# Optimization experiments

Measured on AMD Instinct MI355X. Metric: run time of the kernel, lower is better.

The kernel has to match this reference:

```python
import jax, jax.numpy as jnp
import numpy as np

B, S, D = 2, 2048, 4096
H = 32
HD = D // H  # 128
THETA = 10000.0


def _rope_cos_sin(seq_len, head_dim, theta=THETA):
    # matches precompute_freqs_cis: freqs_cis[t, j] = exp(i * t * theta**(-2j/dim))
    inv = 1.0 / theta ** (np.arange(0, head_dim, 2)[: head_dim // 2].astype(np.float32) / head_dim)
    t = np.arange(seq_len)
    f = np.outer(t, inv).astype(np.float32)  # [S, HD/2]
    return jnp.asarray(np.cos(f)), jnp.asarray(np.sin(f))


def _apply_rotary(x, cos, sin):
    # x: [B, S, H, HD]; interleaved complex rotation as in apply_rotary_emb
    xr = x.astype(jnp.float32).reshape(*x.shape[:-1], HD // 2, 2)
    x0, x1 = xr[..., 0], xr[..., 1]
    c = cos[None, :, None, :]  # [1,S,1,HD/2]
    s = sin[None, :, None, :]
    o0 = x0 * c - x1 * s
    o1 = x0 * s + x1 * c
    return jnp.stack((o0, o1), axis=-1).reshape(*x.shape[:-1], HD)


def setup_inputs() -> dict:
    key = jax.random.key(0)
    ks = jax.random.split(key, 5)
    std = 0.02
    return {
        "x": jax.random.normal(ks[0], (B, S, D), dtype=jnp.float32),
        "wq": jax.random.normal(ks[1], (D, D), dtype=jnp.float32) * std,
        "wk": jax.random.normal(ks[2], (D, D), dtype=jnp.float32) * std,
        "wv": jax.random.normal(ks[3], (D, D), dtype=jnp.float32) * std,
        "wo": jax.random.normal(ks[4], (D, D), dtype=jnp.float32) * std,
    }


def reference(x, wq, wk, wv, wo):
    b, s, d = x.shape
    q = (x @ wq).reshape(b, s, H, HD)
    k = (x @ wk).reshape(b, s, H, HD)
    v = (x @ wv).reshape(b, s, H, HD)

    cos, sin = _rope_cos_sin(s, HD)
    q = _apply_rotary(q, cos, sin)
    k = _apply_rotary(k, cos, sin)

    scale = 1.0 / jnp.sqrt(jnp.float32(HD))
    scores = jnp.einsum("bqhd,bkhd->bhqk", q, k) * scale  # [B,H,S,S]
    causal = jnp.tril(jnp.ones((s, s), dtype=bool))
    scores = jnp.where(causal[None, None], scores, jnp.finfo(scores.dtype).min)
    probs = jax.nn.softmax(scores, axis=-1)
    out = jnp.einsum("bhqk,bkhd->bqhd", probs, v).reshape(b, s, d)
    return out @ wo
```

## Files before the change

kernel.cpp:

```cpp
#include <hip/hip_runtime.h>

#define DEV __device__ __forceinline__
typedef unsigned int u32;
typedef unsigned short u16;
typedef __attribute__((ext_vector_type(8))) __bf16 bf16x8;
typedef __attribute__((ext_vector_type(4))) float f32x4;

#define MFMA16(a,b,c) __builtin_amdgcn_mfma_f32_16x16x32_bf16(a,b,c,0,0,0)

DEV u16 f2bf(float f){ u32 u=__float_as_uint(f); u32 r=(u+0x7fffu+((u>>16)&1u))>>16; return (u16)r; }
DEV float bf2f(u16 h){ return __uint_as_float(((u32)h)<<16); }

DEV void gload16(const void* g, void* l){
  __builtin_amdgcn_global_load_lds((const __attribute__((address_space(1))) void*)g,
                                   (__attribute__((address_space(3))) void*)l, 16, 0, 0);
}


template<bool SPLIT>
__global__ void k_split(const float* __restrict__ in, u16* __restrict__ hi, u16* __restrict__ lo){
  size_t i=((size_t)blockIdx.x*256+threadIdx.x)*4;
  float4 v=*(const float4*)(in+i);
  u16 h0=f2bf(v.x),h1=f2bf(v.y),h2=f2bf(v.z),h3=f2bf(v.w);
  uint2 hh; hh.x=(u32)h0|((u32)h1<<16); hh.y=(u32)h2|((u32)h3<<16);
  *(uint2*)(hi+i)=hh;
  if constexpr(SPLIT){
    uint2 ll; ll.x=(u32)f2bf(v.x-bf2f(h0))|((u32)f2bf(v.y-bf2f(h1))<<16);
    ll.y=(u32)f2bf(v.z-bf2f(h2))|((u32)f2bf(v.w-bf2f(h3))<<16);
    *(uint2*)(lo+i)=ll;
  }
}

template<bool SPLIT>
__global__ void k_trans_split(const float* __restrict__ W, u16* __restrict__ hiT, u16* __restrict__ loT){
  __shared__ float t[64][65];
  const int tid=threadIdx.x;
  const int kb=blockIdx.y*64, nb=blockIdx.x*64;
  for(int p=0;p<4;p++){
    int r=(tid>>4)+p*16, c=(tid&15)*4;
    float4 v=*(const float4*)(W+(size_t)(kb+r)*4096+nb+c);
    t[r][c]=v.x;t[r][c+1]=v.y;t[r][c+2]=v.z;t[r][c+3]=v.w;
  }
  __syncthreads();
  for(int p=0;p<4;p++){
    int orow=(tid>>4)+p*16, oc=(tid&15)*4;
    u16 hs[4],ls[4];
    for(int j=0;j<4;j++){
      float x=t[oc+j][orow];
      hs[j]=f2bf(x); ls[j]=f2bf(x-bf2f(hs[j]));
    }
    uint2 uh; uh.x=(u32)hs[0]|((u32)hs[1]<<16); uh.y=(u32)hs[2]|((u32)hs[3]<<16);
    *(uint2*)(hiT+(size_t)(nb+orow)*4096+kb+oc)=uh;
    if constexpr(SPLIT){
      uint2 ul; ul.x=(u32)ls[0]|((u32)ls[1]<<16); ul.y=(u32)ls[2]|((u32)ls[3]<<16);
      *(uint2*)(loT+(size_t)(nb+orow)*4096+kb+oc)=ul;
    }
  }
}

__global__ void k_rope_tab(float* __restrict__ cosT, float* __restrict__ sinT){
  int i=blockIdx.x*256+threadIdx.x;
  int s=i>>6, f=i&63;
  float inv=powf(10000.f, -(float)(2*f)/128.f);
  float ang=(float)s*inv;
  cosT[i]=cosf(ang); sinT[i]=sinf(ang);
}

template<int EPI, bool SPLIT>
__global__ __launch_bounds__(256,2) void k_gemm(
    const u16* __restrict__ Ah, const u16* __restrict__ Al,
    const u16* __restrict__ Bh, const u16* __restrict__ Bl,
    float* __restrict__ outF, u16* __restrict__ outH, u16* __restrict__ outL,
    const float* __restrict__ cosT, const float* __restrict__ sinT)
{
  __shared__ u16 lds[4][4096];
  const int tid=threadIdx.x, lane=tid&63, w=tid>>6;
  const int m0=blockIdx.y*128, n0=blockIdx.x*128;
  const int wm=(w>>1)*64, wn=(w&1)*64;
  const f32x4 zero4={0.f,0.f,0.f,0.f};
  f32x4 acc[4][4];
  for(int m=0;m<4;m++)for(int n=0;n<4;n++)acc[m][n]=zero4;
  const int srow=lane>>2, soff=(lane&3)*8;
  for(int k0=0;k0<4096;k0+=32){
    for(int q8=w;q8<8;q8+=4){
      int r=q8*16+srow;
      size_t ao=(size_t)(m0+r)*4096+k0+soff;
      size_t bo=(size_t)(n0+r)*4096+k0+soff;
      gload16(Ah+ao,(char*)&lds[0][0]+q8*1024);
      gload16(Bh+bo,(char*)&lds[2][0]+q8*1024);
      if constexpr(SPLIT){
        gload16(Al+ao,(char*)&lds[1][0]+q8*1024);
        gload16(Bl+bo,(char*)&lds[3][0]+q8*1024);
      }
    }
    __syncthreads();
    const int fr=lane&15, fo=(lane>>4)*8;
    bf16x8 ah[4],al[4],bh[4],bl[4];
    for(int m=0;m<4;m++){
      int r=wm+m*16+fr;
      ah[m]=*(const bf16x8*)&lds[0][r*32+fo];
      if constexpr(SPLIT) al[m]=*(const bf16x8*)&lds[1][r*32+fo];
    }
    for(int n=0;n<4;n++){
      int r=wn+n*16+fr;
      bh[n]=*(const bf16x8*)&lds[2][r*32+fo];
      if constexpr(SPLIT) bl[n]=*(const bf16x8*)&lds[3][r*32+fo];
    }
    for(int m=0;m<4;m++)for(int n=0;n<4;n++){
      f32x4 c=acc[m][n];
      c=MFMA16(ah[m],bh[n],c);
      if constexpr(SPLIT){
        c=MFMA16(ah[m],bl[n],c);
        c=MFMA16(al[m],bh[n],c);
      }
      acc[m][n]=c;
    }
    __syncthreads();
  }
  for(int m=0;m<4;m++)for(int n=0;n<4;n++){
    int col=n0+wn+n*16+(lane&15);
    for(int r=0;r<4;r++){
      int row=m0+wm+m*16+(lane>>4)*4+r;
      float v=acc[m][n][r];
      if constexpr(EPI==1){
        int b=row>>11, s=row&2047, hd=col&127, hh=col>>7;
        float part=__shfl_xor(v,1);
        int fi=hd>>1;
        float cs=cosT[s*64+fi], sn=sinT[s*64+fi];
        float o=(hd&1)?(part*sn+v*cs):(v*cs-part*sn);
        u16 hb=f2bf(o);
        size_t addr=((size_t)(b*32+hh)*2048+s)*128+hd;
        outH[addr]=hb;
        if constexpr(SPLIT) outL[addr]=f2bf(o-bf2f(hb));
      } else if constexpr(EPI==2){
        u16 hb=f2bf(v);
        size_t addr=(size_t)row*4096+col;
        outH[addr]=hb;
        if constexpr(SPLIT) outL[addr]=f2bf(v-bf2f(hb));
      } else {
        outF[(size_t)row*4096+col]=v;
      }
    }
  }
}

template<bool SPLIT>
__global__ __launch_bounds__(256,2) void k_attn(
    const u16* __restrict__ Qh, const u16* __restrict__ Ql,
    const u16* __restrict__ Kh, const u16* __restrict__ Kl,
    const u16* __restrict__ VTh, const u16* __restrict__ VTl,
    u16* __restrict__ Oh, u16* __restrict__ Ol)
{
  __shared__ u16 kvh[8192], kvl[8192];
  __shared__ u16 pbuf[4][2][1024];
  const int tid=threadIdx.x, lane=tid&63, w=tid>>6;
  const int q0=blockIdx.x*64, hh=blockIdx.y, b=blockIdx.z;
  const size_t headoff=((size_t)(b*32+hh))*2048*128;
  bf16x8 qh[4],ql[4];
  {
    int qr=q0+w*16+(lane&15);
    for(int c=0;c<4;c++){
      size_t a=headoff+(size_t)qr*128+(lane>>4)*8+32*c;
      qh[c]=*(const bf16x8*)(Qh+a);
      if constexpr(SPLIT) ql[c]=*(const bf16x8*)(Ql+a);
    }
  }
  const f32x4 zero4={0.f,0.f,0.f,0.f};
  f32x4 O[8]; for(int i=0;i<8;i++)O[i]=zero4;
  float m_run=-__builtin_inff(), l_run=0.f;
  const int nt=q0/64+1;
  const int qg=q0+w*16+(lane&15);
  const float scale=0.08838834764831845f;
  for(int t=0;t<nt;t++){
    const int kv0=t*64;
    for(int ch=w*4;ch<w*4+4;++ch){
      int p=ch*1024+lane*16;
      int row=p>>8, slot=(p>>4)&15, ss=slot^(row&7);
      size_t src=headoff+(size_t)(kv0+row)*128+ss*8;
      gload16(Kh+src,(char*)kvh+ch*1024);
      if constexpr(SPLIT) gload16(Kl+src,(char*)kvl+ch*1024);
    }
    __syncthreads();
    f32x4 st[4]; for(int m=0;m<4;m++)st[m]=zero4;
    for(int c=0;c<4;c++){
      for(int m=0;m<4;m++){
        int row=m*16+(lane&15);
        int off=(((lane>>4)*16)+64*c)^((row&7)<<4);
        bf16x8 k8h=*(const bf16x8*)((const char*)kvh+row*256+off);
        st[m]=MFMA16(k8h,qh[c],st[m]);
        if constexpr(SPLIT){
          bf16x8 k8l=*(const bf16x8*)((const char*)kvl+row*256+off);
          st[m]=MFMA16(k8h,ql[c],st[m]);
          st[m]=MFMA16(k8l,qh[c],st[m]);
        }
      }
    }
    __syncthreads();
    for(int ch=w*4;ch<w*4+4;++ch){
      int p=ch*1024+lane*16;
      int row=p>>7, slot=(p>>4)&7, ps=slot^(row&7);
      size_t src=(size_t)(hh*128+row)*4096+(size_t)b*2048+kv0+ps*8;
      gload16(VTh+src,(char*)kvh+ch*1024);
      if constexpr(SPLIT) gload16(VTl+src,(char*)kvl+ch*1024);
    }
    float pm=-__builtin_inff();
    for(int m=0;m<4;m++)for(int r=0;r<4;r++){
      float sv=st[m][r]*scale;
      int kv=kv0+m*16+(lane>>4)*4+r;
      if(kv>qg)sv=-__builtin_inff();
      st[m][r]=sv;
      pm=fmaxf(pm,sv);
    }
    pm=fmaxf(pm,__shfl_xor(pm,16));
    pm=fmaxf(pm,__shfl_xor(pm,32));
    float m_new=fmaxf(m_run,pm);
    float corr=__expf(m_run-m_new);
    float psum=0.f;
    for(int m=0;m<4;m++){
      u16 ph[4],pl[4];
      for(int r=0;r<4;r++){
        float p=__expf(st[m][r]-m_new);
        psum+=p;
        ph[r]=f2bf(p); pl[r]=f2bf(p-bf2f(ph[r]));
      }
      int q=lane&15;
      int off=((m*32)+((lane>>4)*8))^((q&7)<<4);
      uint2 uh; uh.x=(u32)ph[0]|((u32)ph[1]<<16); uh.y=(u32)ph[2]|((u32)ph[3]<<16);
      *(uint2*)((char*)&pbuf[w][0][0]+q*128+off)=uh;
      if constexpr(SPLIT){
        uint2 ul; ul.x=(u32)pl[0]|((u32)pl[1]<<16); ul.y=(u32)pl[2]|((u32)pl[3]<<16);
        *(uint2*)((char*)&pbuf[w][1][0]+q*128+off)=ul;
      }
    }
    psum+=__shfl_xor(psum,16);
    psum+=__shfl_xor(psum,32);
    l_run=l_run*corr+psum;
    m_run=m_new;
    float cb[4];
    for(int r=0;r<4;r++)cb[r]=__shfl(corr,(lane>>4)*4+r);
    for(int nb=0;nb<8;nb++)for(int r=0;r<4;r++)O[nb][r]*=cb[r];
    __syncthreads();
    for(int c2=0;c2<2;c2++){
      int q=lane&15;
      int offp=(((lane>>4)*16)+64*c2)^((q&7)<<4);
      bf16x8 pah=*(const bf16x8*)((const char*)&pbuf[w][0][0]+q*128+offp);
      for(int nb=0;nb<8;nb++){
        int vrow=nb*16+(lane&15);
        int voff=(((lane>>4)*16)+64*c2)^((vrow&7)<<4);
        bf16x8 v8h=*(const bf16x8*)((const char*)kvh+vrow*128+voff);
        O[nb]=MFMA16(pah,v8h,O[nb]);
        if constexpr(SPLIT){
          bf16x8 pal=*(const bf16x8*)((const char*)&pbuf[w][1][0]+q*128+offp);
          bf16x8 v8l=*(const bf16x8*)((const char*)kvl+vrow*128+voff);
          O[nb]=MFMA16(pah,v8l,O[nb]);
          O[nb]=MFMA16(pal,v8h,O[nb]);
        }
      }
    }
    __syncthreads();
  }
  float lb[4];
  for(int r=0;r<4;r++)lb[r]=__shfl(l_run,(lane>>4)*4+r);
  for(int nb=0;nb<8;nb++){
    int col=hh*128+nb*16+(lane&15);
    for(int r=0;r<4;r++){
      float o=O[nb][r]/lb[r];
      size_t rowg=(size_t)b*2048+q0+w*16+(lane>>4)*4+r;
      u16 hb=f2bf(o);
      Oh[rowg*4096+col]=hb;
      if constexpr(SPLIT) Ol[rowg*4096+col]=f2bf(o-bf2f(hb));
    }
  }
}

extern "C" void kernel_launch(void* const* d_in, const int* in_sizes, int n_in,
                              void* d_out, int out_size, void* d_ws, size_t ws_size,
                              hipStream_t stream){
  (void)in_sizes;(void)n_in;(void)out_size;
  const float* x =(const float*)d_in[0];
  const float* wq=(const float*)d_in[1];
  const float* wk=(const float*)d_in[2];
  const float* wv=(const float*)d_in[3];
  const float* wo=(const float*)d_in[4];
  const size_t NELEM=(size_t)4096*4096;
  const size_t MAT=NELEM*sizeof(u16);
  const size_t TAB=(size_t)2048*64*sizeof(float);
  const size_t need_split=10*MAT+2*TAB;
  const size_t need_bf16 = 5*MAT+2*TAB;
  if(ws_size<need_bf16)return;
  const bool split = ws_size>=need_split;
  char* ws=(char*)d_ws;
  size_t off=0;
  auto alloc=[&](size_t bytes)->char*{ char* p=ws+off; off+=bytes; return p; };
  auto allocOpt=[&](size_t bytes)->char*{ if(!split)return nullptr; char* p=ws+off; off+=bytes; return p; };
  u16* x_hi=(u16*)alloc(MAT);   u16* x_lo=(u16*)allocOpt(MAT);
  u16* w_hi=(u16*)alloc(MAT);   u16* w_lo=(u16*)allocOpt(MAT);
  u16* q_hi=(u16*)alloc(MAT);   u16* q_lo=(u16*)allocOpt(MAT);
  u16* k_hi=(u16*)alloc(MAT);   u16* k_lo=(u16*)allocOpt(MAT);
  u16* vT_hi=(u16*)alloc(MAT);  u16* vT_lo=(u16*)allocOpt(MAT);
  float* cosT=(float*)alloc(TAB);
  float* sinT=(float*)alloc(TAB);
  u16* at_hi=x_hi;  u16* at_lo=x_lo;

  dim3 tg(64,64), gg(32,32), ga(32,32,2);
  k_rope_tab<<<512,256,0,stream>>>(cosT,sinT);
  if(split){
    k_split<true><<<(u32)(NELEM/1024),256,0,stream>>>(x,x_hi,x_lo);
    k_trans_split<true><<<tg,256,0,stream>>>(wq,w_hi,w_lo);
    k_gemm<1,true><<<gg,256,0,stream>>>(x_hi,x_lo,w_hi,w_lo,nullptr,q_hi,q_lo,cosT,sinT);
    k_trans_split<true><<<tg,256,0,stream>>>(wk,w_hi,w_lo);
    k_gemm<1,true><<<gg,256,0,stream>>>(x_hi,x_lo,w_hi,w_lo,nullptr,k_hi,k_lo,cosT,sinT);
    k_trans_split<true><<<tg,256,0,stream>>>(wv,w_hi,w_lo);
    k_gemm<2,true><<<gg,256,0,stream>>>(w_hi,w_lo,x_hi,x_lo,nullptr,vT_hi,vT_lo,nullptr,nullptr);
    k_attn<true><<<ga,256,0,stream>>>(q_hi,q_lo,k_hi,k_lo,vT_hi,vT_lo,at_hi,at_lo);
    k_trans_split<true><<<tg,256,0,stream>>>(wo,w_hi,w_lo);
    k_gemm<3,true><<<gg,256,0,stream>>>(at_hi,at_lo,w_hi,w_lo,(float*)d_out,nullptr,nullptr,nullptr,nullptr);
  } else {
    k_split<false><<<(u32)(NELEM/1024),256,0,stream>>>(x,x_hi,nullptr);
    k_trans_split<false><<<tg,256,0,stream>>>(wq,w_hi,nullptr);
    k_gemm<1,false><<<gg,256,0,stream>>>(x_hi,nullptr,w_hi,nullptr,nullptr,q_hi,nullptr,cosT,sinT);
    k_trans_split<false><<<tg,256,0,stream>>>(wk,w_hi,nullptr);
    k_gemm<1,false><<<gg,256,0,stream>>>(x_hi,nullptr,w_hi,nullptr,nullptr,k_hi,nullptr,cosT,sinT);
    k_trans_split<false><<<tg,256,0,stream>>>(wv,w_hi,nullptr);
    k_gemm<2,false><<<gg,256,0,stream>>>(w_hi,nullptr,x_hi,nullptr,nullptr,vT_hi,nullptr,nullptr,nullptr);
    k_attn<false><<<ga,256,0,stream>>>(q_hi,nullptr,k_hi,nullptr,vT_hi,nullptr,at_hi,nullptr);
    k_trans_split<false><<<tg,256,0,stream>>>(wo,w_hi,nullptr);
    k_gemm<3,false><<<gg,256,0,stream>>>(at_hi,nullptr,w_hi,nullptr,(float*)d_out,nullptr,nullptr,nullptr,nullptr);
  }
}
```

Measured before the change: 1.150 ms.

## Replace split-bf16 three-pass MFMA with single-pass fp16 throughout

Drops the hi/lo bf16 split emulation of fp32 and uses plain fp16 operands with a single MFMA per tile in the GEMMs and attention. This cuts matrix-core work, halves LDS and global traffic, and removes the split/residual conversion kernels. The attention kernel also raises its occupancy hint and reverses the query-block order so the longest causal blocks start first. The risk is accuracy: fp16 has fewer mantissa bits than split-bf16 and can overflow on large values.

```diff
diff --git a/kernel.cpp b/kernel.cpp
--- a/kernel.cpp
+++ b/kernel.cpp
@@ -3,13 +3,12 @@
 #define DEV __device__ __forceinline__
 typedef unsigned int u32;
 typedef unsigned short u16;
-typedef __attribute__((ext_vector_type(8))) __bf16 bf16x8;
+typedef __attribute__((ext_vector_type(8))) _Float16 f16x8;
 typedef __attribute__((ext_vector_type(4))) float f32x4;
 
-#define MFMA16(a,b,c) __builtin_amdgcn_mfma_f32_16x16x32_bf16(a,b,c,0,0,0)
-
-DEV u16 f2bf(float f){ u32 u=__float_as_uint(f); u32 r=(u+0x7fffu+((u>>16)&1u))>>16; return (u16)r; }
-DEV float bf2f(u16 h){ return __uint_as_float(((u32)h)<<16); }
+#define MFMA16(a,b,c) __builtin_amdgcn_mfma_f32_16x16x32_f16(a,b,c,0,0,0)
+
+DEV u16 f2h(float f){ _Float16 h=(_Float16)f; return __builtin_bit_cast(u16,h); }
 
 DEV void gload16(const void* g, void* l){
   __builtin_amdgcn_global_load_lds((const __attribute__((address_space(1))) void*)g,
@@ -17,22 +16,14 @@
 }
 
 
-template<bool SPLIT>
-__global__ void k_split(const float* __restrict__ in, u16* __restrict__ hi, u16* __restrict__ lo){
+__global__ void k_cvt(const float* __restrict__ in, u16* __restrict__ out){
   size_t i=((size_t)blockIdx.x*256+threadIdx.x)*4;
   float4 v=*(const float4*)(in+i);
-  u16 h0=f2bf(v.x),h1=f2bf(v.y),h2=f2bf(v.z),h3=f2bf(v.w);
-  uint2 hh; hh.x=(u32)h0|((u32)h1<<16); hh.y=(u32)h2|((u32)h3<<16);
-  *(uint2*)(hi+i)=hh;
-  if constexpr(SPLIT){
-    uint2 ll; ll.x=(u32)f2bf(v.x-bf2f(h0))|((u32)f2bf(v.y-bf2f(h1))<<16);
-    ll.y=(u32)f2bf(v.z-bf2f(h2))|((u32)f2bf(v.w-bf2f(h3))<<16);
-    *(uint2*)(lo+i)=ll;
-  }
-}
-
-template<bool SPLIT>
-__global__ void k_trans_split(const float* __restrict__ W, u16* __restrict__ hiT, u16* __restrict__ loT){
+  uint2 hh; hh.x=(u32)f2h(v.x)|((u32)f2h(v.y)<<16); hh.y=(u32)f2h(v.z)|((u32)f2h(v.w)<<16);
+  *(uint2*)(out+i)=hh;
+}
+
+__global__ void k_trans(const float* __restrict__ W, u16* __restrict__ outT){
   __shared__ float t[64][65];
   const int tid=threadIdx.x;
   const int kb=blockIdx.y*64, nb=blockIdx.x*64;
@@ -44,17 +35,10 @@
   __syncthreads();
   for(int p=0;p<4;p++){
     int orow=(tid>>4)+p*16, oc=(tid&15)*4;
-    u16 hs[4],ls[4];
-    for(int j=0;j<4;j++){
-      float x=t[oc+j][orow];
-      hs[j]=f2bf(x); ls[j]=f2bf(x-bf2f(hs[j]));
-    }
+    u16 hs[4];
+    for(int j=0;j<4;j++) hs[j]=f2h(t[oc+j][orow]);
     uint2 uh; uh.x=(u32)hs[0]|((u32)hs[1]<<16); uh.y=(u32)hs[2]|((u32)hs[3]<<16);
-    *(uint2*)(hiT+(size_t)(nb+orow)*4096+kb+oc)=uh;
-    if constexpr(SPLIT){
-      uint2 ul; ul.x=(u32)ls[0]|((u32)ls[1]<<16); ul.y=(u32)ls[2]|((u32)ls[3]<<16);
-      *(uint2*)(loT+(size_t)(nb+orow)*4096+kb+oc)=ul;
-    }
+    *(uint2*)(outT+(size_t)(nb+orow)*4096+kb+oc)=uh;
   }
 }
 
@@ -66,14 +50,13 @@
   cosT[i]=cosf(ang); sinT[i]=sinf(ang);
 }
 
-template<int EPI, bool SPLIT>
+template<int EPI>
 __global__ __launch_bounds__(256,2) void k_gemm(
-    const u16* __restrict__ Ah, const u16* __restrict__ Al,
-    const u16* __restrict__ Bh, const u16* __restrict__ Bl,
-    float* __restrict__ outF, u16* __restrict__ outH, u16* __restrict__ outL,
+    const u16* __restrict__ A, const u16* __restrict__ B,
+    float* __restrict__ outF, u16* __restrict__ outH,
     const float* __restrict__ cosT, const float* __restrict__ sinT)
 {
-  __shared__ u16 lds[4][4096];
+  __shared__ u16 lds[2][4096];
   const int tid=threadIdx.x, lane=tid&63, w=tid>>6;
   const int m0=blockIdx.y*128, n0=blockIdx.x*128;
   const int wm=(w>>1)*64, wn=(w&1)*64;
@@ -84,37 +67,16 @@
   for(int k0=0;k0<4096;k0+=32){
     for(int q8=w;q8<8;q8+=4){
       int r=q8*16+srow;
-      size_t ao=(size_t)(m0+r)*4096+k0+soff;
-      size_t bo=(size_t)(n0+r)*4096+k0+soff;
-      gload16(Ah+ao,(char*)&lds[0][0]+q8*1024);
-      gload16(Bh+bo,(char*)&lds[2][0]+q8*1024);
-      if constexpr(SPLIT){
-        gload16(Al+ao,(char*)&lds[1][0]+q8*1024);
-        gload16(Bl+bo,(char*)&lds[3][0]+q8*1024);
-      }
+      gload16(A+(size_t)(m0+r)*4096+k0+soff,(char*)&lds[0][0]+q8*1024);
+      gload16(B+(size_t)(n0+r)*4096+k0+soff,(char*)&lds[1][0]+q8*1024);
     }
     __syncthreads();
     const int fr=lane&15, fo=(lane>>4)*8;
-    bf16x8 ah[4],al[4],bh[4],bl[4];
-    for(int m=0;m<4;m++){
-      int r=wm+m*16+fr;
-      ah[m]=*(const bf16x8*)&lds[0][r*32+fo];
-      if constexpr(SPLIT) al[m]=*(const bf16x8*)&lds[1][r*32+fo];
-    }
-    for(int n=0;n<4;n++){
-      int r=wn+n*16+fr;
-      bh[n]=*(const bf16x8*)&lds[2][r*32+fo];
-      if constexpr(SPLIT) bl[n]=*(const bf16x8*)&lds[3][r*32+fo];
-    }
-    for(int m=0;m<4;m++)for(int n=0;n<4;n++){
-      f32x4 c=acc[m][n];
-      c=MFMA16(ah[m],bh[n],c);
-      if constexpr(SPLIT){
-        c=MFMA16(ah[m],bl[n],c);
-        c=MFMA16(al[m],bh[n],c);
-      }
-      acc[m][n]=c;
-    }
+    f16x8 ah[4],bh[4];
+    for(int m=0;m<4;m++) ah[m]=*(const f16x8*)&lds[0][(wm+m*16+fr)*32+fo];
+    for(int n=0;n<4;n++) bh[n]=*(const f16x8*)&lds[1][(wn+n*16+fr)*32+fo];
+    for(int m=0;m<4;m++)for(int n=0;n<4;n++)
+      acc[m][n]=MFMA16(ah[m],bh[n],acc[m][n]);
     __syncthreads();
   }
   for(int m=0;m<4;m++)for(int n=0;n<4;n++){
@@ -128,15 +90,10 @@
         int fi=hd>>1;
         float cs=cosT[s*64+fi], sn=sinT[s*64+fi];
         float o=(hd&1)?(part*sn+v*cs):(v*cs-part*sn);
-        u16 hb=f2bf(o);
         size_t addr=((size_t)(b*32+hh)*2048+s)*128+hd;
-        outH[addr]=hb;
-        if constexpr(SPLIT) outL[addr]=f2bf(o-bf2f(hb));
+        outH[addr]=f2h(o);
       } else if constexpr(EPI==2){
-        u16 hb=f2bf(v);
-        size_t addr=(size_t)row*4096+col;
-        outH[addr]=hb;
-        if constexpr(SPLIT) outL[addr]=f2bf(v-bf2f(hb));
+        outH[(size_t)row*4096+col]=f2h(v);
       } else {
         outF[(size_t)row*4096+col]=v;
       }
@@ -144,26 +101,21 @@
   }
 }
 
-template<bool SPLIT>
-__global__ __launch_bounds__(256,2) void k_attn(
-    const u16* __restrict__ Qh, const u16* __restrict__ Ql,
-    const u16* __restrict__ Kh, const u16* __restrict__ Kl,
-    const u16* __restrict__ VTh, const u16* __restrict__ VTl,
-    u16* __restrict__ Oh, u16* __restrict__ Ol)
+__global__ __launch_bounds__(256,4) void k_attn(
+    const u16* __restrict__ Q, const u16* __restrict__ K,
+    const u16* __restrict__ VT, u16* __restrict__ Oat)
 {
-  __shared__ u16 kvh[8192], kvl[8192];
-  __shared__ u16 pbuf[4][2][1024];
+  __shared__ u16 kv[8192];
+  __shared__ u16 pbuf[4][1024];
   const int tid=threadIdx.x, lane=tid&63, w=tid>>6;
-  const int q0=blockIdx.x*64, hh=blockIdx.y, b=blockIdx.z;
+  const int q0=(31-(int)blockIdx.x)*64;
+  const int hh=blockIdx.y, b=blockIdx.z;
   const size_t headoff=((size_t)(b*32+hh))*2048*128;
-  bf16x8 qh[4],ql[4];
+  f16x8 qh[4];
   {
     int qr=q0+w*16+(lane&15);
-    for(int c=0;c<4;c++){
-      size_t a=headoff+(size_t)qr*128+(lane>>4)*8+32*c;
-      qh[c]=*(const bf16x8*)(Qh+a);
-      if constexpr(SPLIT) ql[c]=*(const bf16x8*)(Ql+a);
-    }
+    for(int c=0;c<4;c++)
+      qh[c]=*(const f16x8*)(Q+headoff+(size_t)qr*128+(lane>>4)*8+32*c);
   }
   const f32x4 zero4={0.f,0.f,0.f,0.f};
   f32x4 O[8]; for(int i=0;i<8;i++)O[i]=zero4;
@@ -176,9 +128,7 @@
     for(int ch=w*4;ch<w*4+4;++ch){
       int p=ch*1024+lane*16;
       int row=p>>8, slot=(p>>4)&15, ss=slot^(row&7);
-      size_t src=headoff+(size_t)(kv0+row)*128+ss*8;
-      gload16(Kh+src,(char*)kvh+ch*1024);
-      if constexpr(SPLIT) gload16(Kl+src,(char*)kvl+ch*1024);
+      gload16(K+headoff+(size_t)(kv0+row)*128+ss*8,(char*)kv+ch*1024);
     }
     __syncthreads();
     f32x4 st[4]; for(int m=0;m<4;m++)st[m]=zero4;
@@ -186,28 +136,21 @@
       for(int m=0;m<4;m++){
         int row=m*16+(lane&15);
         int off=(((lane>>4)*16)+64*c)^((row&7)<<4);
-        bf16x8 k8h=*(const bf16x8*)((const char*)kvh+row*256+off);
-        st[m]=MFMA16(k8h,qh[c],st[m]);
-        if constexpr(SPLIT){
-          bf16x8 k8l=*(const bf16x8*)((const char*)kvl+row*256+off);
-          st[m]=MFMA16(k8h,ql[c],st[m]);
-          st[m]=MFMA16(k8l,qh[c],st[m]);
-        }
+        f16x8 k8=*(const f16x8*)((const char*)kv+row*256+off);
+        st[m]=MFMA16(k8,qh[c],st[m]);
       }
     }
     __syncthreads();
     for(int ch=w*4;ch<w*4+4;++ch){
       int p=ch*1024+lane*16;
       int row=p>>7, slot=(p>>4)&7, ps=slot^(row&7);
-      size_t src=(size_t)(hh*128+row)*4096+(size_t)b*2048+kv0+ps*8;
-      gload16(VTh+src,(char*)kvh+ch*1024);
-      if constexpr(SPLIT) gload16(VTl+src,(char*)kvl+ch*1024);
+      gload16(VT+(size_t)(hh*128+row)*4096+(size_t)b*2048+kv0+ps*8,(char*)kv+ch*1024);
     }
     float pm=-__builtin_inff();
     for(int m=0;m<4;m++)for(int r=0;r<4;r++){
       float sv=st[m][r]*scale;
-      int kv=kv0+m*16+(lane>>4)*4+r;
-      if(kv>qg)sv=-__builtin_inff();
+      int kvi=kv0+m*16+(lane>>4)*4+r;
+      if(kvi>qg)sv=-__builtin_inff();
       st[m][r]=sv;
       pm=fmaxf(pm,sv);
     }
@@ -216,21 +159,17 @@
     float m_new=fmaxf(m_run,pm);
     float corr=__expf(m_run-m_new);
     float psum=0.f;
+    const int q=lane&15;
     for(int m=0;m<4;m++){
-      u16 ph[4],pl[4];
+      u16 ph[4];
       for(int r=0;r<4;r++){
         float p=__expf(st[m][r]-m_new);
         psum+=p;
-        ph[r]=f2bf(p); pl[r]=f2bf(p-bf2f(ph[r]));
-      }
-      int q=lane&15;
+        ph[r]=f2h(p);
+      }
       int off=((m*32)+((lane>>4)*8))^((q&7)<<4);
       uint2 uh; uh.x=(u32)ph[0]|((u32)ph[1]<<16); uh.y=(u32)ph[2]|((u32)ph[3]<<16);
-      *(uint2*)((char*)&pbuf[w][0][0]+q*128+off)=uh;
-      if constexpr(SPLIT){
-        uint2 ul; ul.x=(u32)pl[0]|((u32)pl[1]<<16); ul.y=(u32)pl[2]|((u32)pl[3]<<16);
-        *(uint2*)((char*)&pbuf[w][1][0]+q*128+off)=ul;
-      }
+      *(uint2*)((char*)&pbuf[w][0]+q*128+off)=uh;
     }
     psum+=__shfl_xor(psum,16);
     psum+=__shfl_xor(psum,32);
@@ -241,20 +180,13 @@
     for(int nb=0;nb<8;nb++)for(int r=0;r<4;r++)O[nb][r]*=cb[r];
     __syncthreads();
     for(int c2=0;c2<2;c2++){
-      int q=lane&15;
       int offp=(((lane>>4)*16)+64*c2)^((q&7)<<4);
-      bf16x8 pah=*(const bf16x8*)((const char*)&pbuf[w][0][0]+q*128+offp);
+      f16x8 pa=*(const f16x8*)((const char*)&pbuf[w][0]+q*128+offp);
       for(int nb=0;nb<8;nb++){
         int vrow=nb*16+(lane&15);
         int voff=(((lane>>4)*16)+64*c2)^((vrow&7)<<4);
-        bf16x8 v8h=*(const bf16x8*)((const char*)kvh+vrow*128+voff);
-        O[nb]=MFMA16(pah,v8h,O[nb]);
-        if constexpr(SPLIT){
-          bf16x8 pal=*(const bf16x8*)((const char*)&pbuf[w][1][0]+q*128+offp);
-          bf16x8 v8l=*(const bf16x8*)((const char*)kvl+vrow*128+voff);
-          O[nb]=MFMA16(pah,v8l,O[nb]);
-          O[nb]=MFMA16(pal,v8h,O[nb]);
-        }
+        f16x8 v8=*(const f16x8*)((const char*)kv+vrow*128+voff);
+        O[nb]=MFMA16(pa,v8,O[nb]);
       }
     }
     __syncthreads();
@@ -266,9 +198,7 @@
     for(int r=0;r<4;r++){
       float o=O[nb][r]/lb[r];
       size_t rowg=(size_t)b*2048+q0+w*16+(lane>>4)*4+r;
-      u16 hb=f2bf(o);
-      Oh[rowg*4096+col]=hb;
-      if constexpr(SPLIT) Ol[rowg*4096+col]=f2bf(o-bf2f(hb));
+      Oat[rowg*4096+col]=f2h(o);
     }
   }
 }
@@ -285,46 +215,30 @@
   const size_t NELEM=(size_t)4096*4096;
   const size_t MAT=NELEM*sizeof(u16);
   const size_t TAB=(size_t)2048*64*sizeof(float);
-  const size_t need_split=10*MAT+2*TAB;
-  const size_t need_bf16 = 5*MAT+2*TAB;
-  if(ws_size<need_bf16)return;
-  const bool split = ws_size>=need_split;
+  const size_t need=5*MAT+2*TAB;
+  if(ws_size<need)return;
   char* ws=(char*)d_ws;
   size_t off=0;
   auto alloc=[&](size_t bytes)->char*{ char* p=ws+off; off+=bytes; return p; };
-  auto allocOpt=[&](size_t bytes)->char*{ if(!split)return nullptr; char* p=ws+off; off+=bytes; return p; };
-  u16* x_hi=(u16*)alloc(MAT);   u16* x_lo=(u16*)allocOpt(MAT);
-  u16* w_hi=(u16*)alloc(MAT);   u16* w_lo=(u16*)allocOpt(MAT);
-  u16* q_hi=(u16*)alloc(MAT);   u16* q_lo=(u16*)allocOpt(MAT);
-  u16* k_hi=(u16*)alloc(MAT);   u16* k_lo=(u16*)allocOpt(MAT);
-  u16* vT_hi=(u16*)alloc(MAT);  u16* vT_lo=(u16*)allocOpt(MAT);
+  u16* x_h =(u16*)alloc(MAT);
+  u16* w_h =(u16*)alloc(MAT);
+  u16* q_h =(u16*)alloc(MAT);
+  u16* k_h =(u16*)alloc(MAT);
+  u16* vT_h=(u16*)alloc(MAT);
   float* cosT=(float*)alloc(TAB);
   float* sinT=(float*)alloc(TAB);
-  u16* at_hi=x_hi;  u16* at_lo=x_lo;
+  u16* at_h=x_h;
 
   dim3 tg(64,64), gg(32,32), ga(32,32,2);
   k_rope_tab<<<512,256,0,stream>>>(cosT,sinT);
-  if(split){
-    k_split<true><<<(u32)(NELEM/1024),256,0,stream>>>(x,x_hi,x_lo);
-    k_trans_split<true><<<tg,256,0,stream>>>(wq,w_hi,w_lo);
-    k_gemm<1,true><<<gg,256,0,stream>>>(x_hi,x_lo,w_hi,w_lo,nullptr,q_hi,q_lo,cosT,sinT);
-    k_trans_split<true><<<tg,256,0,stream>>>(wk,w_hi,w_lo);
-    k_gemm<1,true><<<gg,256,0,stream>>>(x_hi,x_lo,w_hi,w_lo,nullptr,k_hi,k_lo,cosT,sinT);
-    k_trans_split<true><<<tg,256,0,stream>>>(wv,w_hi,w_lo);
-    k_gemm<2,true><<<gg,256,0,stream>>>(w_hi,w_lo,x_hi,x_lo,nullptr,vT_hi,vT_lo,nullptr,nullptr);
-    k_attn<true><<<ga,256,0,stream>>>(q_hi,q_lo,k_hi,k_lo,vT_hi,vT_lo,at_hi,at_lo);
-    k_trans_split<true><<<tg,256,0,stream>>>(wo,w_hi,w_lo);
-    k_gemm<3,true><<<gg,256,0,stream>>>(at_hi,at_lo,w_hi,w_lo,(float*)d_out,nullptr,nullptr,nullptr,nullptr);
-  } else {
-    k_split<false><<<(u32)(NELEM/1024),256,0,stream>>>(x,x_hi,nullptr);
-    k_trans_split<false><<<tg,256,0,stream>>>(wq,w_hi,nullptr);
-    k_gemm<1,false><<<gg,256,0,stream>>>(x_hi,nullptr,w_hi,nullptr,nullptr,q_hi,nullptr,cosT,sinT);
-    k_trans_split<false><<<tg,256,0,stream>>>(wk,w_hi,nullptr);
-    k_gemm<1,false><<<gg,256,0,stream>>>(x_hi,nullptr,w_hi,nullptr,nullptr,k_hi,nullptr,cosT,sinT);
-    k_trans_split<false><<<tg,256,0,stream>>>(wv,w_hi,nullptr);
-    k_gemm<2,false><<<gg,256,0,stream>>>(w_hi,nullptr,x_hi,nullptr,nullptr,vT_hi,nullptr,nullptr,nullptr);
-    k_attn<false><<<ga,256,0,stream>>>(q_hi,nullptr,k_hi,nullptr,vT_hi,nullptr,at_hi,nullptr);
-    k_trans_split<false><<<tg,256,0,stream>>>(wo,w_hi,nullptr);
-    k_gemm<3,false><<<gg,256,0,stream>>>(at_hi,nullptr,w_hi,nullptr,(float*)d_out,nullptr,nullptr,nullptr,nullptr);
-  }
-}
+  k_cvt<<<(u32)(NELEM/1024),256,0,stream>>>(x,x_h);
+  k_trans<<<tg,256,0,stream>>>(wq,w_h);
+  k_gemm<1><<<gg,256,0,stream>>>(x_h,w_h,nullptr,q_h,cosT,sinT);
+  k_trans<<<tg,256,0,stream>>>(wk,w_h);
+  k_gemm<1><<<gg,256,0,stream>>>(x_h,w_h,nullptr,k_h,cosT,sinT);
+  k_trans<<<tg,256,0,stream>>>(wv,w_h);
+  k_gemm<2><<<gg,256,0,stream>>>(w_h,x_h,nullptr,vT_h,nullptr,nullptr);
+  k_attn<<<ga,256,0,stream>>>(q_h,k_h,vT_h,at_h);
+  k_trans<<<tg,256,0,stream>>>(wo,w_h);
+  k_gemm<3><<<gg,256,0,stream>>>(at_h,w_h,(float*)d_out,nullptr,nullptr,nullptr);
+}
```

Result: slower. 1.177 ms (+2.4%).
